# Performance work log

Measured on AMD Instinct MI355X. Metric: run time of the kernel, lower is better.

## Reference

```python
import jax, jax.numpy as jnp
import numpy as np

NB, NC, IN, HID, OUT, ENG = 8, 16384, 64, 128, 64, 128
SYNC, DEBATE = 0.15, 0.15


def setup_inputs() -> dict:
    key = jax.random.key(0)
    ks = jax.random.split(key, 24)
    rn = lambda k, s, sc=0.05: jax.random.normal(k, s, jnp.float32) * sc
    return {
        "x": jax.random.normal(ks[0], (1, IN), jnp.float32),
        "noise": jax.random.normal(ks[1], (NB, 1, IN), jnp.float32),
        "amps": jax.random.uniform(ks[2], (NB,), jnp.float32, 0.5, 1.5),
        "hiddens": jax.random.normal(ks[3], (NB, NC, HID), jnp.float32) * 0.1,
        "eaW1": rn(ks[4], (ENG, IN + HID)), "eaB1": rn(ks[5], (ENG,)),
        "eaW2": rn(ks[6], (OUT, ENG)), "eaB2": rn(ks[7], (OUT,)),
        "egW1": rn(ks[8], (ENG, IN + HID)), "egB1": rn(ks[9], (ENG,)),
        "egW2": rn(ks[10], (OUT, ENG)), "egB2": rn(ks[11], (OUT,)),
        "gru_Wih": rn(ks[12], (3 * HID, OUT + 1)), "gru_Whh": rn(ks[13], (3 * HID, HID)),
        "gru_bih": rn(ks[14], (3 * HID,)), "gru_bhh": rn(ks[15], (3 * HID,)),
        "headW": rn(ks[16], (IN, OUT)), "headb": rn(ks[17], (IN,)),
        "mixW": rn(ks[18], (HID, HID * NB)), "mixb": rn(ks[19], (HID,)),
        "step": 10,
    }


def reference(x, noise, amps, hiddens, eaW1, eaB1, eaW2, eaB2,
              egW1, egB1, egW2, egB2, gru_Wih, gru_Whh, gru_bih, gru_bhh,
              headW, headb, mixW, mixb, step):
    sg = jax.lax.stop_gradient
    # per-branch perturbed input, broadcast over cells
    scale = 0.05 * jnp.arange(1, NB + 1, dtype=x.dtype)[:, None, None]
    xb = jnp.broadcast_to(x[None] + noise * scale, (NB, NC, IN))
    comb = jnp.concatenate([xb, hiddens], axis=-1)          # (NB,NC,IN+HID)
    a = jax.nn.relu(comb @ eaW1.T + eaB1) @ eaW2.T + eaB2
    g = jax.nn.relu(comb @ egW1.T + egB1) @ egW2.T + egB2
    out = a - g                                             # (NB,NC,OUT)
    tension = jnp.mean(out ** 2, axis=-1)                   # (NB,NC)

    # GRUCell update (mem input is detached in the original)
    mem_in = sg(jnp.concatenate([out, tension[..., None]], axis=-1))
    gi = mem_in @ gru_Wih.T + gru_bih                       # (NB,NC,3H)
    gh = hiddens @ gru_Whh.T + gru_bhh
    ir, iz, inn = jnp.split(gi, 3, axis=-1)
    hr, hz, hn = jnp.split(gh, 3, axis=-1)
    r = jax.nn.sigmoid(ir + hr)
    z = jax.nn.sigmoid(iz + hz)
    n = jnp.tanh(inn + r * hn)
    newh = sg((1.0 - z) * n + z * hiddens)                  # stored detached

    # faction sync + debate (state only)
    nf = min(8, NC // 2)
    fs = NC // nf
    core = newh[:, :nf * fs].reshape(NB, nf, fs, HID)
    core = (1.0 - SYNC) * core + SYNC * core.mean(axis=2, keepdims=True)
    if step > 5:
        glob = core.mean(axis=2).mean(axis=1)               # (NB,HID)
        dc = max(1, fs // 4)
        core = core.at[:, :, :dc].set(
            (1.0 - DEBATE) * core[:, :, :dc] + DEBATE * glob[:, None, None, :])
    newh = jnp.concatenate([core.reshape(NB, nf * fs, HID), newh[:, nf * fs:]], axis=1)

    # amplitude-weighted branch combine (amps used via .item() -> constants)
    aabs = jnp.abs(amps)
    aabs = aabs / (aabs.sum() + 1e-8)
    cell_out = jnp.einsum('b,bnd->nd', sg(aabs), out)       # (NC,OUT)
    avg_t = tension.mean(axis=0)                            # (NC,)
    w = jax.nn.softmax(sg(avg_t))                           # weights from .item()'d tensions
    combined = (w[:, None] * cell_out).sum(axis=0, keepdims=True)  # (1,OUT)
    pred = combined @ headW.T + headb                       # (1,IN)

    # interference mixer state update on branch 0
    interf = newh.mean(axis=1).reshape(1, -1) @ mixW.T + mixb       # (1,HID)
    newh = newh.at[0].add(sg(interf) * 0.05)

    return pred, avg_t.mean(), newh
```

## Files before the change

### kernel.cpp

```cpp
#include <hip/hip_runtime.h>
#include <math.h>

#define NB   8
#define NCC  16384
#define HID  128

typedef __attribute__((ext_vector_type(8))) short short8;
typedef __attribute__((ext_vector_type(4))) float f32x4;

#define MFMA(a,b,c) __builtin_amdgcn_mfma_f32_16x16x32_bf16(a,b,c,0,0,0)

#define WS_AABS   0
#define WS_BASE1  8
#define WS_BOUT   2056
#define WS_BSUMR  2120
#define WS_BSUMZ  2248
#define WS_BIHN   2376
#define WS_BHHN   2504
#define WS_W64    2632
#define WS_STAT   3016
#define WS_INTERF 3024
#define WS_FRAG   3152
#define WS_SD     64592
#define WS_HM     72784
#define WS_AVGT   73808
#define WS_TS     90192
#define WS_FMEAN  221264
#define WS_GLOB   229456
#define WS_PART2  230480
#define WS_FPART  246864
#define WS_CO     771152

__device__ __forceinline__ unsigned short f2b(float f) {
    unsigned int u = __float_as_uint(f);
    unsigned int r = (u + 0x7fffu + ((u >> 16) & 1u)) >> 16;
    return (unsigned short)r;
}
__device__ __forceinline__ float b2f(unsigned short us) {
    return __uint_as_float(((unsigned int)us) << 16);
}
__device__ __forceinline__ float sigm(float x) {
    return __builtin_amdgcn_rcpf(1.f + __expf(-x));
}
__device__ __forceinline__ float tanh_fast(float x) {
    return 1.f - 2.f * __builtin_amdgcn_rcpf(__expf(2.f * x) + 1.f);
}
__device__ __forceinline__ void stg(char* dst, int row, int cb, float4 u, float4 v) {
    unsigned int p0 = (unsigned)f2b(u.x) | ((unsigned)f2b(u.y) << 16);
    unsigned int p1 = (unsigned)f2b(u.z) | ((unsigned)f2b(u.w) << 16);
    unsigned int p2 = (unsigned)f2b(v.x) | ((unsigned)f2b(v.y) << 16);
    unsigned int p3 = (unsigned)f2b(v.z) | ((unsigned)f2b(v.w) << 16);
    uint4 pk = make_uint4(p0, p1, p2, p3);
    *(uint4*)(dst + row * 256 + (cb ^ ((row & 7) << 4))) = pk;
}

__global__ __launch_bounds__(256) void k0s(
    const float* __restrict__ x, const float* __restrict__ noise,
    const float* __restrict__ amps,
    const float* __restrict__ eaW1, const float* __restrict__ eaB1,
    const float* __restrict__ egW1, const float* __restrict__ egB1,
    const float* __restrict__ eaB2, const float* __restrict__ egB2,
    const float* __restrict__ gbih, const float* __restrict__ gbhh,
    const float* __restrict__ gWih, float* __restrict__ ws)
{
    __shared__ float xb[8][64];
    int t = threadIdx.x;
    for (int i = t; i < 512; i += 256) {
        int b = i >> 6, k = i & 63;
        xb[b][k] = x[k] + noise[b * 64 + k] * (0.05f * (float)(b + 1));
    }
    if (t == 0) {
        float s = 0.f;
        for (int b = 0; b < 8; b++) s += fabsf(amps[b]);
        s += 1e-8f;
        for (int b = 0; b < 8; b++) ws[WS_AABS + b] = fabsf(amps[b]) / s;
    }
    __syncthreads();
    for (int i = t; i < 2048; i += 256) {
        int b = i >> 8, n = i & 255;
        const float* Wp; float s;
        if (n < 128) { Wp = eaW1 + n * 192; s = eaB1[n]; }
        else         { Wp = egW1 + (n - 128) * 192; s = egB1[n - 128]; }
        for (int k = 0; k < 64; k++) s += xb[b][k] * Wp[k];
        ws[WS_BASE1 + i] = s;
    }
    if (t < 64) ws[WS_BOUT + t] = eaB2[t] - egB2[t];
    if (t < 128) {
        ws[WS_BSUMR + t] = gbih[t] + gbhh[t];
        ws[WS_BSUMZ + t] = gbih[128 + t] + gbhh[128 + t];
        ws[WS_BIHN + t]  = gbih[256 + t];
        ws[WS_BHHN + t]  = gbhh[256 + t];
    }
    for (int i = t; i < 384; i += 256) ws[WS_W64 + i] = gWih[i * 65 + 64];
}

__global__ __launch_bounds__(1024) void kfrag(
    const float* __restrict__ eaW1, const float* __restrict__ egW1,
    const float* __restrict__ eaW2, const float* __restrict__ egW2,
    const float* __restrict__ gWih, const float* __restrict__ gWhh,
    float* __restrict__ ws)
{
    int i = blockIdx.x * 1024 + threadIdx.x;
    if (i >= 122880) return;
    short* wsh = (short*)(ws + WS_FRAG);
    float v;
    if (i < 32768) {
        int rel = i;
        int j = rel & 7, l = (rel >> 3) & 63, tk = rel >> 9;
        int kt = tk & 3, nt = tk >> 2;
        int n = nt * 16 + (l & 15), k = kt * 32 + ((l >> 4) << 3) + j;
        v = (n < 128) ? eaW1[n * 192 + 64 + k] : egW1[(n - 128) * 192 + 64 + k];
    } else if (i < 49152) {
        int rel = i - 32768;
        int j = rel & 7, l = (rel >> 3) & 63, tk = rel >> 9;
        int kt = tk & 7, nt = tk >> 3;
        int d = nt * 16 + (l & 15), k = kt * 32 + ((l >> 4) << 3) + j;
        v = (k < 128) ? eaW2[d * 128 + k] : -egW2[d * 128 + (k - 128)];
    } else if (i < 73728) {
        int rel = i - 49152;
        int j = rel & 7, l = (rel >> 3) & 63, tk = rel >> 9;
        int kt = tk & 1, nt = tk >> 1;
        int r = nt * 16 + (l & 15), k = kt * 32 + ((l >> 4) << 3) + j;
        v = gWih[r * 65 + k];
    } else {
        int rel = i - 73728;
        int j = rel & 7, l = (rel >> 3) & 63, tk = rel >> 9;
        int kt = tk & 3, nt = tk >> 2;
        int r = nt * 16 + (l & 15), k = kt * 32 + ((l >> 4) << 3) + j;
        v = gWhh[r * 128 + k];
    }
    wsh[i] = (short)f2b(v);
}

__global__ __launch_bounds__(1024) void kA(
    const float* __restrict__ hiddens, float* __restrict__ newh,
    float* __restrict__ ws)
{
    __shared__ char  wlds[98304];
    __shared__ char  hsb[64 * 256];
    __shared__ char  agb[64 * 512];
    __shared__ float ts_s[64];
    __shared__ float tsum_s[64];

    const int t    = threadIdx.x;
    const int lane = t & 63;
    const int w    = t >> 6;
    const int rg   = w >> 2;
    const int nq   = w & 3;
    const int col  = lane & 15;
    const int kq   = lane >> 4;
    const int r0   = rg * 16;
    const int n0   = blockIdx.x * 64;

    {
        const float4* src = (const float4*)(ws + WS_FRAG);
        float4* dst = (float4*)wlds;
#pragma unroll
        for (int p = 0; p < 6; p++) dst[p * 1024 + t] = src[p * 1024 + t];
    }
    const short8* W1F = (const short8*)wlds;
    const short8* W2F = (const short8*)(wlds + 65536);

    const float bo = ws[WS_BOUT + nq * 16 + col];
    float co_reg[4];
#pragma unroll
    for (int i = 0; i < 4; i++) co_reg[i] = 0.f;
    if (t < 64) tsum_s[t] = 0.f;

    const int flat = t * 8;
    const int srow = flat >> 7;
    const int scb  = (flat & 127) * 2;

    {
        const float* hs = hiddens + (size_t)n0 * HID;
        float4 a0 = *(const float4*)(hs + flat);
        float4 a1 = *(const float4*)(hs + flat + 4);
        stg(hsb, srow, scb, a0, a1);
    }
    float4 pfa0, pfa1;
    unsigned short* outu = (unsigned short*)newh;

    for (int b = 0; b < NB; ++b) {
        __syncthreads();
        if (t < 64) {
            if (b > 0) {
                ws[WS_TS + (size_t)(b - 1) * NCC + n0 + t] = ts_s[t];
                tsum_s[t] += ts_s[t];
            }
            ts_s[t] = 0.f;
        }
        if (b < 7) {
            const float* hsn = hiddens + ((size_t)((b + 1) * NCC + n0)) * HID;
            pfa0 = *(const float4*)(hsn + flat);
            pfa1 = *(const float4*)(hsn + flat + 4);
        }

        {
            short8 aH[4];
#pragma unroll
            for (int ks = 0; ks < 4; ks++) {
                int row = r0 + col;
                aH[ks] = *(const short8*)(hsb + row * 256 +
                           ((ks * 64 + (kq << 4)) ^ ((row & 7) << 4)));
            }
#pragma unroll
            for (int nti = 0; nti < 4; nti++) {
                int nt = nq * 4 + nti;
                f32x4 ac = {0.f, 0.f, 0.f, 0.f};
#pragma unroll
                for (int kt = 0; kt < 4; kt++)
                    ac = MFMA(aH[kt], W1F[(nt * 4 + kt) * 64 + lane], ac);
                int n = nt * 16 + col;
                float bs = ws[WS_BASE1 + b * 256 + n];
#pragma unroll
                for (int j = 0; j < 4; j++) {
                    int row = r0 + (kq << 2) + j;
                    float v = fmaxf(ac[j] + bs, 0.f);
                    *(unsigned short*)(agb + row * 512 +
                        ((n * 2) ^ ((row & 7) << 4))) = f2b(v);
                }
            }
        }
        __syncthreads();

        if (b < 7) stg(hsb, srow, scb, pfa0, pfa1);

        {
            f32x4 ov = {0.f, 0.f, 0.f, 0.f};
#pragma unroll
            for (int kt = 0; kt < 8; kt++) {
                int kb = kt * 64 + (kq << 4);
                int ra = r0 + col;
                short8 a0 = *(const short8*)(agb + ra * 512 + (kb ^ ((ra & 7) << 4)));
                ov = MFMA(a0, W2F[(nq * 8 + kt) * 64 + lane], ov);
            }
            int d = nq * 16 + col;
            float aab = ws[WS_AABS + b];
#pragma unroll
            for (int j = 0; j < 4; j++) {
                int row = r0 + (kq << 2) + j;
                float v = ov[j] + bo;
                co_reg[j] += aab * v;
                outu[(size_t)(b * NCC + n0 + row) * 256 + 192 + d] = f2b(v);
                float sq = v * v;
                sq += __shfl_xor(sq, 1);
                sq += __shfl_xor(sq, 2);
                sq += __shfl_xor(sq, 4);
                sq += __shfl_xor(sq, 8);
                if (col == 0) atomicAdd(&ts_s[row], sq);
            }
        }
    }
    __syncthreads();
    if (t < 64) {
        ws[WS_TS + (size_t)7 * NCC + n0 + t] = ts_s[t];
        tsum_s[t] += ts_s[t];
        ws[WS_AVGT + n0 + t] = tsum_s[t] * (1.f / 512.f);
    }
    {
        int d = nq * 16 + col;
#pragma unroll
        for (int j = 0; j < 4; j++) {
            int row = r0 + (kq << 2) + j;
            ws[WS_CO + (size_t)(n0 + row) * 64 + d] = co_reg[j];
        }
    }
}

__global__ __launch_bounds__(1024) void kB(
    const float* __restrict__ hiddens, float* __restrict__ newh,
    float* __restrict__ ws)
{
    __shared__ char  wl[147456];
    __shared__ char  hsb[32 * 256];
    __shared__ char  otb[32 * 128];
    __shared__ float ts_s[32];
    __shared__ float fp2[2][128];

    const int t    = threadIdx.x;
    const int lane = t & 63;
    const int w    = t >> 6;
    const int rh   = w >> 3;
    const int hg   = w & 7;
    const int col  = lane & 15;
    const int kq   = lane >> 4;
    const int chunk = blockIdx.x;
    const int n0   = chunk * 32;

    {
        const float4* src = (const float4*)(ws + WS_FRAG) + 6144;
        float4* dst = (float4*)wl;
#pragma unroll
        for (int p = 0; p < 9; p++) dst[p * 1024 + t] = src[p * 1024 + t];
    }
    const short8* WIHF = (const short8*)wl;
    const short8* WHHF = (const short8*)(wl + 49152);
    const unsigned short* outu = (const unsigned short*)newh;

    const int h = hg * 16 + col;
    const float bsr = ws[WS_BSUMR + h];
    const float bsz = ws[WS_BSUMZ + h];
    const float bin = ws[WS_BIHN + h];
    const float bhn = ws[WS_BHHN + h];
    const float wr  = ws[WS_W64 + h];
    const float wz  = ws[WS_W64 + 128 + h];
    const float wn  = ws[WS_W64 + 256 + h];

    const int flat = t * 8;
    const int srow = flat >> 7;
    const int scb  = (flat & 127) * 2;
    const int ocell = t >> 4;
    const int ooff  = (t & 15) * 4;

    float4 rh0 = {0,0,0,0}, rh1 = {0,0,0,0};
    uint2  ro = make_uint2(0, 0);
    float  rts = 0.f;
    if (t < 512) {
        const float* hs = hiddens + (size_t)n0 * HID;
        rh0 = *(const float4*)(hs + flat);
        rh1 = *(const float4*)(hs + flat + 4);
        ro  = *(const uint2*)(outu + (size_t)(n0 + ocell) * 256 + 192 + ooff);
    }
    if (t < 32) rts = ws[WS_TS + n0 + t];

    for (int b = 0; b < NB; ++b) {
        if (t < 512) {
            stg(hsb, srow, scb, rh0, rh1);
            *(uint2*)(otb + ocell * 128 + ((ooff * 2) ^ ((ocell & 7) << 4))) = ro;
        }
        if (t < 32) ts_s[t] = rts;
        __syncthreads();

        if (b < 7) {
            if (t < 512) {
                const float* hsn = hiddens + ((size_t)((b + 1) * NCC + n0)) * HID;
                rh0 = *(const float4*)(hsn + flat);
                rh1 = *(const float4*)(hsn + flat + 4);
                ro  = *(const uint2*)(outu + (size_t)((b + 1) * NCC + n0 + ocell) * 256 + 192 + ooff);
            }
            if (t < 32) rts = ws[WS_TS + (size_t)(b + 1) * NCC + n0 + t];
        }

        {
            float* nbase = newh + ((size_t)(b * NCC + n0)) * HID;
            const int ra = rh * 16 + col;
            f32x4 R = {0.f,0.f,0.f,0.f};
            f32x4 Z = {0.f,0.f,0.f,0.f};
            f32x4 I = {0.f,0.f,0.f,0.f};
            f32x4 N = {0.f,0.f,0.f,0.f};
#pragma unroll
            for (int ks = 0; ks < 2; ks++) {
                short8 a0 = *(const short8*)(otb + ra * 128 +
                             ((ks * 64 + (kq << 4)) ^ ((ra & 7) << 4)));
                R = MFMA(a0, WIHF[(hg * 2 + ks) * 64 + lane], R);
                Z = MFMA(a0, WIHF[((hg + 8) * 2 + ks) * 64 + lane], Z);
                I = MFMA(a0, WIHF[((hg + 16) * 2 + ks) * 64 + lane], I);
            }
#pragma unroll
            for (int ks = 0; ks < 4; ks++) {
                short8 a0 = *(const short8*)(hsb + ra * 256 +
                             ((ks * 64 + (kq << 4)) ^ ((ra & 7) << 4)));
                R = MFMA(a0, WHHF[(hg * 4 + ks) * 64 + lane], R);
                Z = MFMA(a0, WHHF[((hg + 8) * 4 + ks) * 64 + lane], Z);
                N = MFMA(a0, WHHF[((hg + 16) * 4 + ks) * 64 + lane], N);
            }
            float flsum = 0.f;
#pragma unroll
            for (int j = 0; j < 4; j++) {
                int row = rh * 16 + (kq << 2) + j;
                float tv = ts_s[row] * (1.f / 64.f);
                float r  = sigm(R[j] + bsr + tv * wr);
                float z  = sigm(Z[j] + bsz + tv * wz);
                float hn = N[j] + bhn;
                float nn = tanh_fast(I[j] + bin + tv * wn + r * hn);
                float hold = b2f(*(const unsigned short*)(hsb + row * 256 +
                                 ((h * 2) ^ ((row & 7) << 4))));
                float nh = (1.f - z) * nn + z * hold;
                nbase[(size_t)row * HID + h] = nh;
                flsum += nh;
            }
            flsum += __shfl_xor(flsum, 16);
            flsum += __shfl_xor(flsum, 32);
            if (kq == 0) fp2[rh][h] = flsum;
        }
        __syncthreads();

        if (t < 128)
            ws[WS_FPART + ((size_t)(b * 512 + chunk)) * 128 + t] = fp2[0][t] + fp2[1][t];
    }
}

__global__ __launch_bounds__(128) void k2_fmean(float* __restrict__ ws)
{
    int bf = blockIdx.x;
    int b = bf >> 3, f = bf & 7;
    int h = threadIdx.x;
    float s = 0.f, s8 = 0.f;
    for (int j = 0; j < 64; j++) {
        float v = ws[WS_FPART + ((size_t)(b * 512 + f * 64 + j)) * 128 + h];
        s += v;
        if (j < 16) s8 += v;
    }
    ws[WS_FMEAN + (b * 8 + f) * 128 + h] = s * (1.f / 2048.f);
    ws[WS_SD + (b * 8 + f) * 128 + h] = s8;
}

__global__ __launch_bounds__(1024) void k4gh(
    const int* __restrict__ step, float* __restrict__ ws)
{
    int t = threadIdx.x;
    int b = t >> 7, h = t & 127;
    float s = 0.f;
    for (int f = 0; f < 8; f++) s += ws[WS_FMEAN + (b * 8 + f) * 128 + h];
    float gl = s * 0.125f;
    ws[WS_GLOB + t] = gl;
    float tot = 16384.f * gl;
    if (step[0] > 5) {
        float sd = 0.f;
        for (int f = 0; f < 8; f++) sd += ws[WS_SD + (b * 8 + f) * 128 + h];
        tot += 0.15f * (3481.6f * gl - 0.85f * sd);
    }
    ws[WS_HM + t] = tot * (1.f / 16384.f);
}

__global__ __launch_bounds__(256) void k4mv(
    const float* __restrict__ mixW, const float* __restrict__ mixb,
    float* __restrict__ ws)
{
    __shared__ float red[256];
    int h = blockIdx.x, t = threadIdx.x;
    float4 wv = *(const float4*)(mixW + (size_t)h * 1024 + t * 4);
    float4 hv = *(const float4*)(ws + WS_HM + t * 4);
    float s = wv.x * hv.x + wv.y * hv.y + wv.z * hv.z + wv.w * hv.w;
    red[t] = s; __syncthreads();
    for (int st = 128; st > 0; st >>= 1) { if (t < st) red[t] += red[t + st]; __syncthreads(); }
    if (t == 0) ws[WS_INTERF + h] = mixb[h] + red[0];
}

__global__ __launch_bounds__(256) void k35_blend(
    float* __restrict__ newh, const float* __restrict__ ws,
    const int* __restrict__ step)
{
    int blk = blockIdx.x;
    int b = blk >> 8, ck = blk & 255;
    int t = threadIdx.x;
    int h = t & 127, half = t >> 7;
    int base = ck * 64 + half * 32;
    int f = ck >> 5;
    bool deb = (step[0] > 5) && (((ck * 64) & 2047) < 512);
    float fm  = ws[WS_FMEAN + (b * 8 + f) * 128 + h];
    float gl  = ws[WS_GLOB + b * 128 + h];
    float itf = (b == 0) ? 0.05f * ws[WS_INTERF + h] : 0.f;
    for (int i = 0; i < 32; i++) {
        size_t idx = ((size_t)b * NCC + base + i) * HID + h;
        float v = newh[idx];
        v = 0.85f * v + 0.15f * fm;
        if (deb) v = 0.85f * v + 0.15f * gl;
        newh[idx] = v + itf;
    }
}

__global__ __launch_bounds__(1024) void kstat(float* __restrict__ ws, float* __restrict__ d_out)
{
    __shared__ float red[1024];
    __shared__ float msh;
    int t = threadIdx.x;
    float mx = -3.4e38f, sm = 0.f;
    for (int n = t; n < NCC; n += 1024) {
        float v = ws[WS_AVGT + n];
        mx = fmaxf(mx, v);
        sm += v;
    }
    red[t] = mx; __syncthreads();
    for (int st = 512; st > 0; st >>= 1) { if (t < st) red[t] = fmaxf(red[t], red[t + st]); __syncthreads(); }
    if (t == 0) msh = red[0];
    __syncthreads();
    float m = msh;
    red[t] = sm; __syncthreads();
    for (int st = 512; st > 0; st >>= 1) { if (t < st) red[t] += red[t + st]; __syncthreads(); }
    if (t == 0) d_out[64] = red[0] * (1.f / (float)NCC);
    __syncthreads();
    float se = 0.f;
    for (int n = t; n < NCC; n += 1024) se += __expf(ws[WS_AVGT + n] - m);
    red[t] = se; __syncthreads();
    for (int st = 512; st > 0; st >>= 1) { if (t < st) red[t] += red[t + st]; __syncthreads(); }
    if (t == 0) { ws[WS_STAT] = m; ws[WS_STAT + 1] = red[0]; }
}

__global__ __launch_bounds__(256) void kred(float* __restrict__ ws)
{
    __shared__ float wexp[64];
    __shared__ float red[256];
    int blk = blockIdx.x, t = threadIdx.x;
    int n0 = blk * 64;
    float m = ws[WS_STAT];
    if (t < 64) wexp[t] = __expf(ws[WS_AVGT + n0 + t] - m);
    __syncthreads();
    int d = t & 63, q = t >> 6;
    float s = 0.f;
    for (int i = 0; i < 16; i++) {
        int c = q * 16 + i;
        s += wexp[c] * ws[WS_CO + (size_t)(n0 + c) * 64 + d];
    }
    red[t] = s; __syncthreads();
    if (t < 64)
        ws[WS_PART2 + blk * 64 + t] = red[t] + red[64 + t] + red[128 + t] + red[192 + t];
}

__global__ __launch_bounds__(256) void kpred(
    const float* __restrict__ headW, const float* __restrict__ headb,
    float* __restrict__ ws, float* __restrict__ d_out)
{
    __shared__ float red[256];
    __shared__ float comb[64];
    int t = threadIdx.x;
    int d = t & 63, q = t >> 6;
    float s = 0.f;
    for (int i = 0; i < 64; i++) s += ws[WS_PART2 + (q * 64 + i) * 64 + d];
    red[t] = s; __syncthreads();
    if (t < 64) comb[t] = (red[t] + red[64 + t] + red[128 + t] + red[192 + t]) / ws[WS_STAT + 1];
    __syncthreads();
    if (t < 64) {
        float p = headb[t];
        for (int d2 = 0; d2 < 64; d2++) p += comb[d2] * headW[t * 64 + d2];
        d_out[t] = p;
    }
}

extern "C" void kernel_launch(void* const* d_in, const int* in_sizes, int n_in,
                              void* d_out, int out_size, void* d_ws, size_t ws_size,
                              hipStream_t stream)
{
    const float* x       = (const float*)d_in[0];
    const float* noise   = (const float*)d_in[1];
    const float* amps    = (const float*)d_in[2];
    const float* hiddens = (const float*)d_in[3];
    const float* eaW1    = (const float*)d_in[4];
    const float* eaB1    = (const float*)d_in[5];
    const float* eaW2    = (const float*)d_in[6];
    const float* eaB2    = (const float*)d_in[7];
    const float* egW1    = (const float*)d_in[8];
    const float* egB1    = (const float*)d_in[9];
    const float* egW2    = (const float*)d_in[10];
    const float* egB2    = (const float*)d_in[11];
    const float* gWih    = (const float*)d_in[12];
    const float* gWhh    = (const float*)d_in[13];
    const float* gbih    = (const float*)d_in[14];
    const float* gbhh    = (const float*)d_in[15];
    const float* headW   = (const float*)d_in[16];
    const float* headb   = (const float*)d_in[17];
    const float* mixW    = (const float*)d_in[18];
    const float* mixb    = (const float*)d_in[19];
    const int*   step    = (const int*)d_in[20];

    float* out  = (float*)d_out;
    float* newh = out + 65;
    float* ws   = (float*)d_ws;

    k0s<<<1, 256, 0, stream>>>(x, noise, amps, eaW1, eaB1, egW1, egB1,
                               eaB2, egB2, gbih, gbhh, gWih, ws);
    kfrag<<<120, 1024, 0, stream>>>(eaW1, egW1, eaW2, egW2, gWih, gWhh, ws);
    kA<<<256, 1024, 0, stream>>>(hiddens, newh, ws);
    kB<<<512, 1024, 0, stream>>>(hiddens, newh, ws);
    k2_fmean<<<64, 128, 0, stream>>>(ws);
    k4gh<<<1, 1024, 0, stream>>>(step, ws);
    k4mv<<<128, 256, 0, stream>>>(mixW, mixb, ws);
    k35_blend<<<2048, 256, 0, stream>>>(newh, ws, step);
    kstat<<<1, 1024, 0, stream>>>(ws, out);
    kred<<<256, 256, 0, stream>>>(ws);
    kpred<<<1, 256, 0, stream>>>(headW, headb, ws, out);
}
```

Measured before the change: 140.5 us.

## Fuse small prep and reduction kernels, drop softmax max pass, vectorize blend

Merges the scalar prep kernel into the weight-fragment kernel, folds the global-mean computation into the mixer matvec, and removes the separate softmax statistics kernel. It does this by computing exp(avg_t) without max subtraction, with per-block partial sums reduced in the final prediction kernel. The blend kernel now uses float4 loads and stores and recomputes the global mean locally. A packed bf16 conversion instruction replaces the manual rounding. Together these cut launches and serial single-block kernels, but the unshifted exp could overflow if tensions were large, and the mixer blocks now redundantly recompute the 1024-entry mean.

Result: faster. 131.2 us (-6.7%).

```diff
diff --git a/kernel.cpp b/kernel.cpp
--- a/kernel.cpp
+++ b/kernel.cpp
@@ -18,18 +18,17 @@
 #define WS_BIHN   2376
 #define WS_BHHN   2504
 #define WS_W64    2632
-#define WS_STAT   3016
 #define WS_INTERF 3024
 #define WS_FRAG   3152
 #define WS_SD     64592
-#define WS_HM     72784
 #define WS_AVGT   73808
 #define WS_TS     90192
 #define WS_FMEAN  221264
-#define WS_GLOB   229456
 #define WS_PART2  230480
 #define WS_FPART  246864
 #define WS_CO     771152
+#define WS_PARTE  1819728
+#define WS_PARTA  1819984
 
 __device__ __forceinline__ unsigned short f2b(float f) {
     unsigned int u = __float_as_uint(f);
@@ -45,91 +44,90 @@
 __device__ __forceinline__ float tanh_fast(float x) {
     return 1.f - 2.f * __builtin_amdgcn_rcpf(__expf(2.f * x) + 1.f);
 }
+__device__ __forceinline__ unsigned int cvtpk(float lo, float hi) {
+    unsigned int r;
+    asm volatile("v_cvt_pk_bf16_f32 %0, %1, %2" : "=v"(r) : "v"(lo), "v"(hi));
+    return r;
+}
 __device__ __forceinline__ void stg(char* dst, int row, int cb, float4 u, float4 v) {
-    unsigned int p0 = (unsigned)f2b(u.x) | ((unsigned)f2b(u.y) << 16);
-    unsigned int p1 = (unsigned)f2b(u.z) | ((unsigned)f2b(u.w) << 16);
-    unsigned int p2 = (unsigned)f2b(v.x) | ((unsigned)f2b(v.y) << 16);
-    unsigned int p3 = (unsigned)f2b(v.z) | ((unsigned)f2b(v.w) << 16);
-    uint4 pk = make_uint4(p0, p1, p2, p3);
+    uint4 pk = make_uint4(cvtpk(u.x, u.y), cvtpk(u.z, u.w),
+                          cvtpk(v.x, v.y), cvtpk(v.z, v.w));
     *(uint4*)(dst + row * 256 + (cb ^ ((row & 7) << 4))) = pk;
 }
 
-__global__ __launch_bounds__(256) void k0s(
+__global__ __launch_bounds__(1024) void kprep(
     const float* __restrict__ x, const float* __restrict__ noise,
     const float* __restrict__ amps,
     const float* __restrict__ eaW1, const float* __restrict__ eaB1,
     const float* __restrict__ egW1, const float* __restrict__ egB1,
-    const float* __restrict__ eaB2, const float* __restrict__ egB2,
+    const float* __restrict__ eaW2, const float* __restrict__ eaB2,
+    const float* __restrict__ egW2, const float* __restrict__ egB2,
+    const float* __restrict__ gWih, const float* __restrict__ gWhh,
     const float* __restrict__ gbih, const float* __restrict__ gbhh,
-    const float* __restrict__ gWih, float* __restrict__ ws)
-{
-    __shared__ float xb[8][64];
-    int t = threadIdx.x;
-    for (int i = t; i < 512; i += 256) {
-        int b = i >> 6, k = i & 63;
-        xb[b][k] = x[k] + noise[b * 64 + k] * (0.05f * (float)(b + 1));
-    }
-    if (t == 0) {
-        float s = 0.f;
-        for (int b = 0; b < 8; b++) s += fabsf(amps[b]);
-        s += 1e-8f;
-        for (int b = 0; b < 8; b++) ws[WS_AABS + b] = fabsf(amps[b]) / s;
-    }
-    __syncthreads();
-    for (int i = t; i < 2048; i += 256) {
-        int b = i >> 8, n = i & 255;
-        const float* Wp; float s;
-        if (n < 128) { Wp = eaW1 + n * 192; s = eaB1[n]; }
-        else         { Wp = egW1 + (n - 128) * 192; s = egB1[n - 128]; }
-        for (int k = 0; k < 64; k++) s += xb[b][k] * Wp[k];
-        ws[WS_BASE1 + i] = s;
-    }
-    if (t < 64) ws[WS_BOUT + t] = eaB2[t] - egB2[t];
-    if (t < 128) {
-        ws[WS_BSUMR + t] = gbih[t] + gbhh[t];
-        ws[WS_BSUMZ + t] = gbih[128 + t] + gbhh[128 + t];
-        ws[WS_BIHN + t]  = gbih[256 + t];
-        ws[WS_BHHN + t]  = gbhh[256 + t];
-    }
-    for (int i = t; i < 384; i += 256) ws[WS_W64 + i] = gWih[i * 65 + 64];
-}
-
-__global__ __launch_bounds__(1024) void kfrag(
-    const float* __restrict__ eaW1, const float* __restrict__ egW1,
-    const float* __restrict__ eaW2, const float* __restrict__ egW2,
-    const float* __restrict__ gWih, const float* __restrict__ gWhh,
     float* __restrict__ ws)
 {
     int i = blockIdx.x * 1024 + threadIdx.x;
-    if (i >= 122880) return;
-    short* wsh = (short*)(ws + WS_FRAG);
-    float v;
-    if (i < 32768) {
-        int rel = i;
-        int j = rel & 7, l = (rel >> 3) & 63, tk = rel >> 9;
-        int kt = tk & 3, nt = tk >> 2;
-        int n = nt * 16 + (l & 15), k = kt * 32 + ((l >> 4) << 3) + j;
-        v = (n < 128) ? eaW1[n * 192 + 64 + k] : egW1[(n - 128) * 192 + 64 + k];
-    } else if (i < 49152) {
-        int rel = i - 32768;
-        int j = rel & 7, l = (rel >> 3) & 63, tk = rel >> 9;
-        int kt = tk & 7, nt = tk >> 3;
-        int d = nt * 16 + (l & 15), k = kt * 32 + ((l >> 4) << 3) + j;
-        v = (k < 128) ? eaW2[d * 128 + k] : -egW2[d * 128 + (k - 128)];
-    } else if (i < 73728) {
-        int rel = i - 49152;
-        int j = rel & 7, l = (rel >> 3) & 63, tk = rel >> 9;
-        int kt = tk & 1, nt = tk >> 1;
-        int r = nt * 16 + (l & 15), k = kt * 32 + ((l >> 4) << 3) + j;
-        v = gWih[r * 65 + k];
-    } else {
-        int rel = i - 73728;
-        int j = rel & 7, l = (rel >> 3) & 63, tk = rel >> 9;
-        int kt = tk & 3, nt = tk >> 2;
-        int r = nt * 16 + (l & 15), k = kt * 32 + ((l >> 4) << 3) + j;
-        v = gWhh[r * 128 + k];
-    }
-    wsh[i] = (short)f2b(v);
+    if (i < 122880) {
+        short* wsh = (short*)(ws + WS_FRAG);
+        float v;
+        if (i < 32768) {
+            int rel = i;
+            int j = rel & 7, l = (rel >> 3) & 63, tk = rel >> 9;
+            int kt = tk & 3, nt = tk >> 2;
+            int n = nt * 16 + (l & 15), k = kt * 32 + ((l >> 4) << 3) + j;
+            v = (n < 128) ? eaW1[n * 192 + 64 + k] : egW1[(n - 128) * 192 + 64 + k];
+        } else if (i < 49152) {
+            int rel = i - 32768;
+            int j = rel & 7, l = (rel >> 3) & 63, tk = rel >> 9;
+            int kt = tk & 7, nt = tk >> 3;
+            int d = nt * 16 + (l & 15), k = kt * 32 + ((l >> 4) << 3) + j;
+            v = (k < 128) ? eaW2[d * 128 + k] : -egW2[d * 128 + (k - 128)];
+        } else if (i < 73728) {
+            int rel = i - 49152;
+            int j = rel & 7, l = (rel >> 3) & 63, tk = rel >> 9;
+            int kt = tk & 1, nt = tk >> 1;
+            int r = nt * 16 + (l & 15), k = kt * 32 + ((l >> 4) << 3) + j;
+            v = gWih[r * 65 + k];
+        } else {
+            int rel = i - 73728;
+            int j = rel & 7, l = (rel >> 3) & 63, tk = rel >> 9;
+            int kt = tk & 3, nt = tk >> 2;
+            int r = nt * 16 + (l & 15), k = kt * 32 + ((l >> 4) << 3) + j;
+            v = gWhh[r * 128 + k];
+        }
+        wsh[i] = (short)f2b(v);
+    }
+    if (blockIdx.x == 0) {
+        __shared__ float xb[8][64];
+        int t = threadIdx.x;
+        if (t < 512) {
+            int b = t >> 6, k = t & 63;
+            xb[b][k] = x[k] + noise[b * 64 + k] * (0.05f * (float)(b + 1));
+        }
+        if (t == 0) {
+            float s = 0.f;
+            for (int b = 0; b < 8; b++) s += fabsf(amps[b]);
+            s += 1e-8f;
+            for (int b = 0; b < 8; b++) ws[WS_AABS + b] = fabsf(amps[b]) / s;
+        }
+        __syncthreads();
+        for (int ii = t; ii < 2048; ii += 1024) {
+            int b = ii >> 8, n = ii & 255;
+            const float* Wp; float s;
+            if (n < 128) { Wp = eaW1 + n * 192; s = eaB1[n]; }
+            else         { Wp = egW1 + (n - 128) * 192; s = egB1[n - 128]; }
+            for (int k = 0; k < 64; k++) s += xb[b & 7][k] * Wp[k];
+            ws[WS_BASE1 + ii] = s;
+        }
+        if (t < 64) ws[WS_BOUT + t] = eaB2[t] - egB2[t];
+        if (t < 128) {
+            ws[WS_BSUMR + t] = gbih[t] + gbhh[t];
+            ws[WS_BSUMZ + t] = gbih[128 + t] + gbhh[128 + t];
+            ws[WS_BIHN + t]  = gbih[256 + t];
+            ws[WS_BHHN + t]  = gbhh[256 + t];
+        }
+        if (t < 384) ws[WS_W64 + t] = gWih[t * 65 + 64];
+    }
 }
 
 __global__ __launch_bounds__(1024) void kA(
@@ -405,36 +403,33 @@
     ws[WS_SD + (b * 8 + f) * 128 + h] = s8;
 }
 
-__global__ __launch_bounds__(1024) void k4gh(
-    const int* __restrict__ step, float* __restrict__ ws)
-{
-    int t = threadIdx.x;
-    int b = t >> 7, h = t & 127;
-    float s = 0.f;
-    for (int f = 0; f < 8; f++) s += ws[WS_FMEAN + (b * 8 + f) * 128 + h];
-    float gl = s * 0.125f;
-    ws[WS_GLOB + t] = gl;
-    float tot = 16384.f * gl;
-    if (step[0] > 5) {
-        float sd = 0.f;
-        for (int f = 0; f < 8; f++) sd += ws[WS_SD + (b * 8 + f) * 128 + h];
-        tot += 0.15f * (3481.6f * gl - 0.85f * sd);
-    }
-    ws[WS_HM + t] = tot * (1.f / 16384.f);
-}
-
 __global__ __launch_bounds__(256) void k4mv(
     const float* __restrict__ mixW, const float* __restrict__ mixb,
-    float* __restrict__ ws)
-{
+    const int* __restrict__ step, float* __restrict__ ws)
+{
+    __shared__ float hm[1024];
     __shared__ float red[256];
-    int h = blockIdx.x, t = threadIdx.x;
-    float4 wv = *(const float4*)(mixW + (size_t)h * 1024 + t * 4);
-    float4 hv = *(const float4*)(ws + WS_HM + t * 4);
+    int h0 = blockIdx.x, t = threadIdx.x;
+    bool deb = (step[0] > 5);
+    for (int j = t; j < 1024; j += 256) {
+        int b = j >> 7, hh = j & 127;
+        float s = 0.f, sd = 0.f;
+        for (int f = 0; f < 8; f++) {
+            s  += ws[WS_FMEAN + (b * 8 + f) * 128 + hh];
+            sd += ws[WS_SD + (b * 8 + f) * 128 + hh];
+        }
+        float gl = s * 0.125f;
+        float tot = 16384.f * gl;
+        if (deb) tot += 0.15f * (3481.6f * gl - 0.85f * sd);
+        hm[j] = tot * (1.f / 16384.f);
+    }
+    __syncthreads();
+    float4 wv = *(const float4*)(mixW + (size_t)h0 * 1024 + t * 4);
+    float4 hv = *(const float4*)(&hm[t * 4]);
     float s = wv.x * hv.x + wv.y * hv.y + wv.z * hv.z + wv.w * hv.w;
     red[t] = s; __syncthreads();
     for (int st = 128; st > 0; st >>= 1) { if (t < st) red[t] += red[t + st]; __syncthreads(); }
-    if (t == 0) ws[WS_INTERF + h] = mixb[h] + red[0];
+    if (t == 0) ws[WS_INTERF + h0] = mixb[h0] + red[0];
 }
 
 __global__ __launch_bounds__(256) void k35_blend(
@@ -444,47 +439,41 @@
     int blk = blockIdx.x;
     int b = blk >> 8, ck = blk & 255;
     int t = threadIdx.x;
-    int h = t & 127, half = t >> 7;
-    int base = ck * 64 + half * 32;
-    int f = ck >> 5;
-    bool deb = (step[0] > 5) && (((ck * 64) & 2047) < 512);
-    float fm  = ws[WS_FMEAN + (b * 8 + f) * 128 + h];
-    float gl  = ws[WS_GLOB + b * 128 + h];
-    float itf = (b == 0) ? 0.05f * ws[WS_INTERF + h] : 0.f;
-    for (int i = 0; i < 32; i++) {
-        size_t idx = ((size_t)b * NCC + base + i) * HID + h;
-        float v = newh[idx];
-        v = 0.85f * v + 0.15f * fm;
-        if (deb) v = 0.85f * v + 0.15f * gl;
-        newh[idx] = v + itf;
-    }
-}
-
-__global__ __launch_bounds__(1024) void kstat(float* __restrict__ ws, float* __restrict__ d_out)
-{
-    __shared__ float red[1024];
-    __shared__ float msh;
-    int t = threadIdx.x;
-    float mx = -3.4e38f, sm = 0.f;
-    for (int n = t; n < NCC; n += 1024) {
-        float v = ws[WS_AVGT + n];
-        mx = fmaxf(mx, v);
-        sm += v;
-    }
-    red[t] = mx; __syncthreads();
-    for (int st = 512; st > 0; st >>= 1) { if (t < st) red[t] = fmaxf(red[t], red[t + st]); __syncthreads(); }
-    if (t == 0) msh = red[0];
-    __syncthreads();
-    float m = msh;
-    red[t] = sm; __syncthreads();
-    for (int st = 512; st > 0; st >>= 1) { if (t < st) red[t] += red[t + st]; __syncthreads(); }
-    if (t == 0) d_out[64] = red[0] * (1.f / (float)NCC);
-    __syncthreads();
-    float se = 0.f;
-    for (int n = t; n < NCC; n += 1024) se += __expf(ws[WS_AVGT + n] - m);
-    red[t] = se; __syncthreads();
-    for (int st = 512; st > 0; st >>= 1) { if (t < st) red[t] += red[t + st]; __syncthreads(); }
-    if (t == 0) { ws[WS_STAT] = m; ws[WS_STAT + 1] = red[0]; }
+    int h4 = t & 31;
+    int cg = t >> 5;
+    int base = ck * 64;
+    int f = base >> 11;
+    bool deb = (step[0] > 5) && ((base & 2047) < 512);
+    float4 fm = *(const float4*)(ws + WS_FMEAN + (size_t)(b * 8 + f) * 128 + h4 * 4);
+    float glx = 0.f, gly = 0.f, glz = 0.f, glw = 0.f;
+    for (int ff = 0; ff < 8; ff++) {
+        float4 v = *(const float4*)(ws + WS_FMEAN + (size_t)(b * 8 + ff) * 128 + h4 * 4);
+        glx += v.x; gly += v.y; glz += v.z; glw += v.w;
+    }
+    glx *= 0.125f; gly *= 0.125f; glz *= 0.125f; glw *= 0.125f;
+    float4 itf = {0.f, 0.f, 0.f, 0.f};
+    if (b == 0) {
+        float4 iv = *(const float4*)(ws + WS_INTERF + h4 * 4);
+        itf.x = 0.05f * iv.x; itf.y = 0.05f * iv.y;
+        itf.z = 0.05f * iv.z; itf.w = 0.05f * iv.w;
+    }
+    for (int i = 0; i < 8; i++) {
+        int cell = base + i * 8 + cg;
+        size_t idx = ((size_t)b * NCC + cell) * 128 + h4 * 4;
+        float4 v = *(float4*)(newh + idx);
+        v.x = 0.85f * v.x + 0.15f * fm.x;
+        v.y = 0.85f * v.y + 0.15f * fm.y;
+        v.z = 0.85f * v.z + 0.15f * fm.z;
+        v.w = 0.85f * v.w + 0.15f * fm.w;
+        if (deb) {
+            v.x = 0.85f * v.x + 0.15f * glx;
+            v.y = 0.85f * v.y + 0.15f * gly;
+            v.z = 0.85f * v.z + 0.15f * glz;
+            v.w = 0.85f * v.w + 0.15f * glw;
+        }
+        v.x += itf.x; v.y += itf.y; v.z += itf.z; v.w += itf.w;
+        *(float4*)(newh + idx) = v;
+    }
 }
 
 __global__ __launch_bounds__(256) void kred(float* __restrict__ ws)
@@ -493,8 +482,11 @@
     __shared__ float red[256];
     int blk = blockIdx.x, t = threadIdx.x;
     int n0 = blk * 64;
-    float m = ws[WS_STAT];
-    if (t < 64) wexp[t] = __expf(ws[WS_AVGT + n0 + t] - m);
+    float av = 0.f;
+    if (t < 64) {
+        av = ws[WS_AVGT + n0 + t];
+        wexp[t] = __expf(av);
+    }
     __syncthreads();
     int d = t & 63, q = t >> 6;
     float s = 0.f;
@@ -505,6 +497,16 @@
     red[t] = s; __syncthreads();
     if (t < 64)
         ws[WS_PART2 + blk * 64 + t] = red[t] + red[64 + t] + red[128 + t] + red[192 + t];
+    if (t < 64) {
+        float e = wexp[t], a2 = av;
+        e  += __shfl_xor(e, 1);  a2 += __shfl_xor(a2, 1);
+        e  += __shfl_xor(e, 2);  a2 += __shfl_xor(a2, 2);
+        e  += __shfl_xor(e, 4);  a2 += __shfl_xor(a2, 4);
+        e  += __shfl_xor(e, 8);  a2 += __shfl_xor(a2, 8);
+        e  += __shfl_xor(e, 16); a2 += __shfl_xor(a2, 16);
+        e  += __shfl_xor(e, 32); a2 += __shfl_xor(a2, 32);
+        if (t == 0) { ws[WS_PARTE + blk] = e; ws[WS_PARTA + blk] = a2; }
+    }
 }
 
 __global__ __launch_bounds__(256) void kpred(
@@ -512,17 +514,27 @@
     float* __restrict__ ws, float* __restrict__ d_out)
 {
     __shared__ float red[256];
-    __shared__ float comb[64];
+    __shared__ float num[64];
+    __shared__ float den_s;
     int t = threadIdx.x;
     int d = t & 63, q = t >> 6;
     float s = 0.f;
     for (int i = 0; i < 64; i++) s += ws[WS_PART2 + (q * 64 + i) * 64 + d];
     red[t] = s; __syncthreads();
-    if (t < 64) comb[t] = (red[t] + red[64 + t] + red[128 + t] + red[192 + t]) / ws[WS_STAT + 1];
+    if (t < 64) num[t] = red[t] + red[64 + t] + red[128 + t] + red[192 + t];
+    __syncthreads();
+    red[t] = ws[WS_PARTE + t]; __syncthreads();
+    for (int st = 128; st > 0; st >>= 1) { if (t < st) red[t] += red[t + st]; __syncthreads(); }
+    if (t == 0) den_s = red[0];
+    __syncthreads();
+    red[t] = ws[WS_PARTA + t]; __syncthreads();
+    for (int st = 128; st > 0; st >>= 1) { if (t < st) red[t] += red[t + st]; __syncthreads(); }
+    if (t == 0) d_out[64] = red[0] * (1.f / (float)NCC);
     __syncthreads();
     if (t < 64) {
+        float inv_den = 1.f / den_s;
         float p = headb[t];
-        for (int d2 = 0; d2 < 64; d2++) p += comb[d2] * headW[t * 64 + d2];
+        for (int d2 = 0; d2 < 64; d2++) p += (num[d2] * inv_den) * headW[t * 64 + d2];
         d_out[t] = p;
     }
 }
@@ -557,16 +569,14 @@
     float* newh = out + 65;
     float* ws   = (float*)d_ws;
 
-    k0s<<<1, 256, 0, stream>>>(x, noise, amps, eaW1, eaB1, egW1, egB1,
-                               eaB2, egB2, gbih, gbhh, gWih, ws);
-    kfrag<<<120, 1024, 0, stream>>>(eaW1, egW1, eaW2, egW2, gWih, gWhh, ws);
+    kprep<<<120, 1024, 0, stream>>>(x, noise, amps, eaW1, eaB1, egW1, egB1,
+                                    eaW2, eaB2, egW2, egB2, gWih, gWhh,
+                                    gbih, gbhh, ws);
     kA<<<256, 1024, 0, stream>>>(hiddens, newh, ws);
     kB<<<512, 1024, 0, stream>>>(hiddens, newh, ws);
     k2_fmean<<<64, 128, 0, stream>>>(ws);
-    k4gh<<<1, 1024, 0, stream>>>(step, ws);
-    k4mv<<<128, 256, 0, stream>>>(mixW, mixb, ws);
+    k4mv<<<128, 256, 0, stream>>>(mixW, mixb, step, ws);
     k35_blend<<<2048, 256, 0, stream>>>(newh, ws, step);
-    kstat<<<1, 1024, 0, stream>>>(ws, out);
     kred<<<256, 256, 0, stream>>>(ws);
     kpred<<<1, 256, 0, stream>>>(headW, headb, ws, out);
 }
```
